# Kernel optimization log

Measured on AMD Instinct MI355X. Metric: run time of the kernel, lower is better.

## Reference

```python
import jax, jax.numpy as jnp
import numpy as np

NTOKENS = 50257
NHID = 1024
NTOK_PER_CLASS = 225   # ceil(sqrt(50257))
NCLASSES = 224         # ceil(50257/225)
BATCH = 2048


def setup_inputs() -> dict:
    key = jax.random.key(0)
    k1, k2, k3, k4 = jax.random.split(key, 4)
    initrange = 0.1
    inputs = jax.random.normal(k1, (BATCH, NHID), dtype=jnp.float32)
    labels = jax.random.randint(k2, (BATCH,), 0, NTOKENS, dtype=jnp.int64)
    layer_top_W = jax.random.uniform(k3, (NHID, NCLASSES), dtype=jnp.float32,
                                     minval=-initrange, maxval=initrange)
    layer_top_b = jnp.zeros((NCLASSES,), dtype=jnp.float32)
    layer_bottom_W = jax.random.uniform(k4, (NCLASSES, NHID, NTOK_PER_CLASS),
                                        dtype=jnp.float32,
                                        minval=-initrange, maxval=initrange)
    layer_bottom_b = jnp.zeros((NCLASSES, NTOK_PER_CLASS), dtype=jnp.float32)
    return {"inputs": inputs, "labels": labels,
            "layer_top_W": layer_top_W, "layer_top_b": layer_top_b,
            "layer_bottom_W": layer_bottom_W, "layer_bottom_b": layer_bottom_b}


def reference(inputs, labels, layer_top_W, layer_top_b, layer_bottom_W, layer_bottom_b):
    batch_size = inputs.shape[0]
    label_position_top = labels // NTOK_PER_CLASS          # [B]
    label_position_bottom = labels % NTOK_PER_CLASS        # [B]

    # top-level class probabilities
    top_logits = inputs @ layer_top_W + layer_top_b        # [B, nclasses]
    top_probs = jax.nn.softmax(top_logits, axis=1)

    # per-sample gather of class weight matrices + batched matmul
    W_sel = layer_bottom_W[label_position_top]             # [B, nhid, ntok_per_class]
    b_sel = layer_bottom_b[label_position_top]             # [B, ntok_per_class]
    bottom_logits = jnp.einsum('bh,bht->bt', inputs, W_sel) + b_sel
    bottom_probs = jax.nn.softmax(bottom_logits, axis=1)

    idx = jnp.arange(batch_size)
    target_probs = top_probs[idx, label_position_top] * bottom_probs[idx, label_position_bottom]
    return target_probs
```

## Files before the change

### kernel.cpp

```cpp
#include <hip/hip_runtime.h>
#include <math.h>

#define NHID  1024
#define NCLS  224
#define NTPC  225
#define BATCH 2048
#define XP    18

#define NBOT_BLOCKS (NCLS * 4)
#define NTOP_BLOCKS (128 * 4)

#define CLS_OFF  0
#define POS_OFF  8192
#define LIST_OFF 16384
#define OFFS_OFF 24576
#define YTOP_OFF 32768
#define YTOP_BYTES (BATCH * NCLS * 4)
#define YBOT_OFF (YTOP_OFF + YTOP_BYTES)
#define YBOT_BYTES (BATCH * NTPC * 4)

__global__ __launch_bounds__(256) void group_kernel(const int* __restrict__ labels,
                                                    int* __restrict__ cls,
                                                    int* __restrict__ pos,
                                                    int* __restrict__ list,
                                                    int* __restrict__ offs) {
    __shared__ int cnt[NCLS];
    __shared__ int sc[256];
    __shared__ int bex[NCLS];
    __shared__ int nz;
    const int tid = threadIdx.x;
    if (tid == 0) nz = 0;
    for (int j = tid; j < NCLS; j += 256) cnt[j] = 0;
    __syncthreads();
    int loc = 0;
    for (int k = 0; k < 4; ++k) {
        int i = tid + 256 * k;
        if (labels[2 * i + 1] != 0) loc = 1;
    }
    if (loc) atomicOr(&nz, 1);
    __syncthreads();
    const bool is64 = (nz == 0);
    int myc[8], myr[8];
#pragma unroll
    for (int k = 0; k < 8; ++k) {
        int i = tid + 256 * k;
        int l = is64 ? labels[2 * i] : labels[i];
        int c = l / NTPC;
        cls[i] = c;
        pos[i] = l - c * NTPC;
        myc[k] = c;
        myr[k] = atomicAdd(&cnt[c], 1);
    }
    __syncthreads();
    int v = (tid < NCLS) ? cnt[tid] : 0;
    sc[tid] = v;
    __syncthreads();
    for (int off = 1; off < 256; off <<= 1) {
        int u = (tid >= off) ? sc[tid - off] : 0;
        __syncthreads();
        sc[tid] += u;
        __syncthreads();
    }
    if (tid < NCLS) {
        int ex = sc[tid] - v;
        bex[tid] = ex;
        offs[tid] = ex;
    }
    if (tid == 0) offs[NCLS] = BATCH;
    __syncthreads();
#pragma unroll
    for (int k = 0; k < 8; ++k) {
        int i = tid + 256 * k;
        list[bex[myc[k]] + myr[k]] = i;
    }
}

__global__ __launch_bounds__(256) void partial_kernel(const float* __restrict__ x,
                                                      const float* __restrict__ Wt,
                                                      const float* __restrict__ Wb,
                                                      const int* __restrict__ list,
                                                      const int* __restrict__ offs,
                                                      float* __restrict__ ytop,
                                                      float* __restrict__ ybot) {
    __shared__ __align__(16) float xs[256 * XP];
    const int tid = threadIdx.x;
    const int w = tid >> 6, l = tid & 63;
    const int bi = blockIdx.x;
    const bool isBot = (bi < NBOT_BLOCKS);

    int k, o, n, ycols;
    const float* W;
    float* y;
    if (isBot) {
        int c = bi >> 2; k = bi & 3;
        o = offs[c]; n = offs[c + 1] - o;
        W = Wb + (size_t)c * (NHID * NTPC);
        y = ybot; ycols = NTPC;
    } else {
        int b2 = bi - NBOT_BLOCKS;
        int st = b2 >> 2; k = b2 & 3;
        o = st * 16; n = 16;
        W = Wt; y = ytop; ycols = NCLS;
    }
    const int hbase = k * 256;

    for (int tile = 0; tile * 16 < n; ++tile) {
        if (tile) __syncthreads();
        for (int i = 0; i < 16; ++i) {
            int idx = tile * 16 + i;
            int s = isBot ? list[o + min(idx, n - 1)] : (o + i);
            xs[tid * XP + i] = x[(size_t)s * NHID + hbase + tid];
        }
        __syncthreads();
        const int nt = min(n - tile * 16, 16);
        if (4 * w < nt) {
            float acc[4][4];
#pragma unroll
            for (int m = 0; m < 4; ++m)
#pragma unroll
                for (int g = 0; g < 4; ++g) acc[m][g] = 0.f;
            const float* wr = W + (size_t)hbase * ycols + l;
#pragma unroll 4
            for (int h = 0; h < 256; ++h) {
                float2 xa = *(const float2*)&xs[h * XP + 4 * w];
                float2 xb = *(const float2*)&xs[h * XP + 4 * w + 2];
                float wv[4];
                wv[0] = wr[0];
                wv[1] = wr[64];
                wv[2] = wr[128];
                wv[3] = (192 + l < ycols) ? wr[192] : 0.f;
                const float xm[4] = {xa.x, xa.y, xb.x, xb.y};
#pragma unroll
                for (int m = 0; m < 4; ++m)
#pragma unroll
                    for (int g = 0; g < 4; ++g)
                        acc[m][g] = fmaf(xm[m], wv[g], acc[m][g]);
                wr += ycols;
            }
            const int smax = min(nt - 4 * w, 4);
            for (int m = 0; m < smax; ++m) {
                int idx = tile * 16 + 4 * w + m;
                int s = isBot ? list[o + idx] : (o + 4 * w + m);
                float* yr = y + (size_t)s * ycols;
#pragma unroll
                for (int g = 0; g < 4; ++g) {
                    int col = l + 64 * g;
                    if (col < ycols) atomicAdd(&yr[col], acc[m][g]);
                }
            }
        }
    }
}

__global__ __launch_bounds__(256) void finalize_kernel(const float* __restrict__ ytop,
                                                       const float* __restrict__ ybot,
                                                       const float* __restrict__ bt,
                                                       const float* __restrict__ bb,
                                                       const int* __restrict__ cls,
                                                       const int* __restrict__ pos,
                                                       float* __restrict__ out) {
    const int w = threadIdx.x >> 6, l = threadIdx.x & 63;
    const int s = blockIdx.x * 4 + w;
    const int c = cls[s], p = pos[s];

    float v[4];
#pragma unroll
    for (int g = 0; g < 4; ++g) {
        int col = l + 64 * g;
        v[g] = (col < NCLS) ? ytop[(size_t)s * NCLS + col] + bt[col] : -INFINITY;
    }
    float mx = fmaxf(fmaxf(v[0], v[1]), fmaxf(v[2], v[3]));
#pragma unroll
    for (int off = 32; off; off >>= 1) mx = fmaxf(mx, __shfl_xor(mx, off));
    float sum = 0.f, tc = 0.f;
#pragma unroll
    for (int g = 0; g < 4; ++g) {
        int col = l + 64 * g;
        float e = (col < NCLS) ? __expf(v[g] - mx) : 0.f;
        sum += e;
        if (col == c) tc = e;
    }
#pragma unroll
    for (int off = 32; off; off >>= 1) {
        sum += __shfl_xor(sum, off);
        tc  += __shfl_xor(tc, off);
    }
    const float tp = tc / sum;

#pragma unroll
    for (int g = 0; g < 4; ++g) {
        int col = l + 64 * g;
        v[g] = (col < NTPC) ? ybot[(size_t)s * NTPC + col] + bb[c * NTPC + col] : -INFINITY;
    }
    mx = fmaxf(fmaxf(v[0], v[1]), fmaxf(v[2], v[3]));
#pragma unroll
    for (int off = 32; off; off >>= 1) mx = fmaxf(mx, __shfl_xor(mx, off));
    float bsum = 0.f;
    float ep = 0.f;
#pragma unroll
    for (int g = 0; g < 4; ++g) {
        int col = l + 64 * g;
        float e = (col < NTPC) ? __expf(v[g] - mx) : 0.f;
        bsum += e;
        if (col == p) ep = e;
    }
#pragma unroll
    for (int off = 32; off; off >>= 1) bsum += __shfl_xor(bsum, off);
    if (ep != 0.f || (l == (p & 63) && (l + 64 * (p >> 6) == p)))
        ;
    int owner = ((l + 64 * 0 == p) || (l + 64 * 1 == p) || (l + 64 * 2 == p) || (l + 64 * 3 == p));
    if (owner) out[s] = tp * ep / bsum;
}

extern "C" void kernel_launch(void* const* d_in, const int* in_sizes, int n_in,
                              void* d_out, int out_size, void* d_ws, size_t ws_size,
                              hipStream_t stream) {
    const float* inputs = (const float*)d_in[0];
    const int*   labels = (const int*)d_in[1];
    const float* topW   = (const float*)d_in[2];
    const float* topB   = (const float*)d_in[3];
    const float* botW   = (const float*)d_in[4];
    const float* botB   = (const float*)d_in[5];
    float* out = (float*)d_out;

    char* ws   = (char*)d_ws;
    int*   cls = (int*)(ws + CLS_OFF);
    int*   pos = (int*)(ws + POS_OFF);
    int*   lst = (int*)(ws + LIST_OFF);
    int*   off = (int*)(ws + OFFS_OFF);
    float* ytop = (float*)(ws + YTOP_OFF);
    float* ybot = (float*)(ws + YBOT_OFF);

    hipMemsetAsync(ws + YTOP_OFF, 0, YTOP_BYTES + YBOT_BYTES, stream);
    group_kernel<<<1, 256, 0, stream>>>(labels, cls, pos, lst, off);
    partial_kernel<<<NBOT_BLOCKS + NTOP_BLOCKS, 256, 0, stream>>>(
        inputs, topW, botW, lst, off, ytop, ybot);
    finalize_kernel<<<BATCH / 4, 256, 0, stream>>>(ytop, ybot, topB, botB, cls, pos, out);
}
```

Measured before the change: 344.4 us.

## Remap partial GEMM threads to one column by sixteen samples with swizzled LDS

```diff
diff --git a/kernel.cpp b/kernel.cpp
--- a/kernel.cpp
+++ b/kernel.cpp
@@ -5,7 +5,6 @@
 #define NCLS  224
 #define NTPC  225
 #define BATCH 2048
-#define XP    18
 
 #define NBOT_BLOCKS (NCLS * 4)
 #define NTOP_BLOCKS (128 * 4)
@@ -82,7 +81,7 @@
                                                       const int* __restrict__ offs,
                                                       float* __restrict__ ytop,
                                                       float* __restrict__ ybot) {
-    __shared__ __align__(16) float xs[256 * XP];
+    __shared__ __align__(16) float xs[256 * 16];
     const int tid = threadIdx.x;
     const int w = tid >> 6, l = tid & 63;
     const int bi = blockIdx.x;
@@ -103,50 +102,60 @@
         W = Wt; y = ytop; ycols = NCLS;
     }
     const int hbase = k * 256;
+    const int col   = 64 * w + l;
+    const int colc  = min(col, ycols - 1);
+    const bool colok = (col < ycols);
+    const int hq = (tid >> 1) & 3;
 
     for (int tile = 0; tile * 16 < n; ++tile) {
         if (tile) __syncthreads();
+        const float* xcol = x + hbase + tid;
+#pragma unroll
         for (int i = 0; i < 16; ++i) {
             int idx = tile * 16 + i;
             int s = isBot ? list[o + min(idx, n - 1)] : (o + i);
-            xs[tid * XP + i] = x[(size_t)s * NHID + hbase + tid];
+            xs[(tid << 4) + ((((i >> 2) ^ hq) << 2) | (i & 3))] = xcol[(size_t)s * NHID];
         }
         __syncthreads();
+
+        float acc[16];
+#pragma unroll
+        for (int i = 0; i < 16; ++i) acc[i] = 0.f;
+
+        const float* wr = W + (size_t)hbase * ycols + colc;
+#pragma unroll 8
+        for (int h = 0; h < 256; ++h) {
+            float wv = wr[0];
+            const float4* xr = (const float4*)&xs[h << 4];
+            const int q = (h >> 1) & 3;
+            float4 x0 = xr[q];
+            float4 x1 = xr[1 ^ q];
+            float4 x2 = xr[2 ^ q];
+            float4 x3 = xr[3 ^ q];
+            acc[0]  = fmaf(x0.x, wv, acc[0]);
+            acc[1]  = fmaf(x0.y, wv, acc[1]);
+            acc[2]  = fmaf(x0.z, wv, acc[2]);
+            acc[3]  = fmaf(x0.w, wv, acc[3]);
+            acc[4]  = fmaf(x1.x, wv, acc[4]);
+            acc[5]  = fmaf(x1.y, wv, acc[5]);
+            acc[6]  = fmaf(x1.z, wv, acc[6]);
+            acc[7]  = fmaf(x1.w, wv, acc[7]);
+            acc[8]  = fmaf(x2.x, wv, acc[8]);
+            acc[9]  = fmaf(x2.y, wv, acc[9]);
+            acc[10] = fmaf(x2.z, wv, acc[10]);
+            acc[11] = fmaf(x2.w, wv, acc[11]);
+            acc[12] = fmaf(x3.x, wv, acc[12]);
+            acc[13] = fmaf(x3.y, wv, acc[13]);
+            acc[14] = fmaf(x3.z, wv, acc[14]);
+            acc[15] = fmaf(x3.w, wv, acc[15]);
+            wr += ycols;
+        }
+
         const int nt = min(n - tile * 16, 16);
-        if (4 * w < nt) {
-            float acc[4][4];
-#pragma unroll
-            for (int m = 0; m < 4; ++m)
-#pragma unroll
-                for (int g = 0; g < 4; ++g) acc[m][g] = 0.f;
-            const float* wr = W + (size_t)hbase * ycols + l;
-#pragma unroll 4
-            for (int h = 0; h < 256; ++h) {
-                float2 xa = *(const float2*)&xs[h * XP + 4 * w];
-                float2 xb = *(const float2*)&xs[h * XP + 4 * w + 2];
-                float wv[4];
-                wv[0] = wr[0];
-                wv[1] = wr[64];
-                wv[2] = wr[128];
-                wv[3] = (192 + l < ycols) ? wr[192] : 0.f;
-                const float xm[4] = {xa.x, xa.y, xb.x, xb.y};
-#pragma unroll
-                for (int m = 0; m < 4; ++m)
-#pragma unroll
-                    for (int g = 0; g < 4; ++g)
-                        acc[m][g] = fmaf(xm[m], wv[g], acc[m][g]);
-                wr += ycols;
-            }
-            const int smax = min(nt - 4 * w, 4);
-            for (int m = 0; m < smax; ++m) {
-                int idx = tile * 16 + 4 * w + m;
-                int s = isBot ? list[o + idx] : (o + 4 * w + m);
-                float* yr = y + (size_t)s * ycols;
-#pragma unroll
-                for (int g = 0; g < 4; ++g) {
-                    int col = l + 64 * g;
-                    if (col < ycols) atomicAdd(&yr[col], acc[m][g]);
-                }
+        if (colok) {
+            for (int i = 0; i < nt; ++i) {
+                int s = isBot ? list[o + tile * 16 + i] : (o + i);
+                atomicAdd(&y[(size_t)s * ycols + col], acc[i]);
             }
         }
     }
@@ -195,8 +204,7 @@
     mx = fmaxf(fmaxf(v[0], v[1]), fmaxf(v[2], v[3]));
 #pragma unroll
     for (int off = 32; off; off >>= 1) mx = fmaxf(mx, __shfl_xor(mx, off));
-    float bsum = 0.f;
-    float ep = 0.f;
+    float bsum = 0.f, ep = 0.f;
 #pragma unroll
     for (int g = 0; g < 4; ++g) {
         int col = l + 64 * g;
@@ -206,10 +214,11 @@
     }
 #pragma unroll
     for (int off = 32; off; off >>= 1) bsum += __shfl_xor(bsum, off);
-    if (ep != 0.f || (l == (p & 63) && (l + 64 * (p >> 6) == p)))
-        ;
-    int owner = ((l + 64 * 0 == p) || (l + 64 * 1 == p) || (l + 64 * 2 == p) || (l + 64 * 3 == p));
-    if (owner) out[s] = tp * ep / bsum;
+    int owner = ((l == (p & 63)) && ((p >> 6) == ((l + 64 * ((p >> 6))) == p ? (p >> 6) : -1)));
+#pragma unroll
+    for (int g = 0; g < 4; ++g)
+        if (l + 64 * g == p) out[s] = tp * ep / bsum;
+    (void)owner;
 }
 
 extern "C" void kernel_launch(void* const* d_in, const int* in_sizes, int n_in,
```

New measurement: 344.3 us. About the same (-0.0%).

## Split hidden dimension across waves instead of samples in partial matmul kernel

Applied to the files above, without the earlier changes.

```diff
diff --git a/kernel.cpp b/kernel.cpp
--- a/kernel.cpp
+++ b/kernel.cpp
@@ -5,7 +5,6 @@
 #define NCLS  224
 #define NTPC  225
 #define BATCH 2048
-#define XP    18
 
 #define NBOT_BLOCKS (NCLS * 4)
 #define NTOP_BLOCKS (128 * 4)
@@ -75,14 +74,49 @@
     }
 }
 
-__global__ __launch_bounds__(256) void partial_kernel(const float* __restrict__ x,
-                                                      const float* __restrict__ Wt,
-                                                      const float* __restrict__ Wb,
-                                                      const int* __restrict__ list,
-                                                      const int* __restrict__ offs,
-                                                      float* __restrict__ ytop,
-                                                      float* __restrict__ ybot) {
-    __shared__ __align__(16) float xs[256 * XP];
+template <int NQ>
+__device__ __forceinline__ void pk_compute(const float* __restrict__ wr0,
+                                           const float* __restrict__ xs,
+                                           float acc[NQ][4][4],
+                                           int ycols, int hw, int l) {
+#pragma unroll
+    for (int q = 0; q < NQ; ++q)
+#pragma unroll
+        for (int m = 0; m < 4; ++m)
+#pragma unroll
+            for (int g = 0; g < 4; ++g) acc[q][m][g] = 0.f;
+    const float* wr = wr0;
+#pragma unroll 4
+    for (int h = 0; h < 64; ++h) {
+        const int hh = hw + h;
+        float wv[4];
+        wv[0] = wr[0];
+        wv[1] = wr[64];
+        wv[2] = wr[128];
+        wv[3] = wr[192 + l < ycols ? 192 : 0];
+        const int sw = (hh >> 1) & 3;
+#pragma unroll
+        for (int q = 0; q < NQ; ++q) {
+            float4 xq = *(const float4*)&xs[(hh << 4) + 4 * (q ^ sw)];
+            const float xm[4] = {xq.x, xq.y, xq.z, xq.w};
+#pragma unroll
+            for (int m = 0; m < 4; ++m)
+#pragma unroll
+                for (int g = 0; g < 4; ++g)
+                    acc[q][m][g] = fmaf(xm[m], wv[g], acc[q][m][g]);
+        }
+        wr += ycols;
+    }
+}
+
+__global__ __launch_bounds__(256, 4) void partial_kernel(const float* __restrict__ x,
+                                                         const float* __restrict__ Wt,
+                                                         const float* __restrict__ Wb,
+                                                         const int* __restrict__ list,
+                                                         const int* __restrict__ offs,
+                                                         float* __restrict__ ytop,
+                                                         float* __restrict__ ybot) {
+    __shared__ __align__(16) float xs[256 * 16];
     const int tid = threadIdx.x;
     const int w = tid >> 6, l = tid & 63;
     const int bi = blockIdx.x;
@@ -103,49 +137,42 @@
         W = Wt; y = ytop; ycols = NCLS;
     }
     const int hbase = k * 256;
+    const int hw = 64 * w;
+    const int hq = (tid >> 1) & 3;
+    const float* wr0 = W + (size_t)(hbase + hw) * ycols + l;
 
     for (int tile = 0; tile * 16 < n; ++tile) {
         if (tile) __syncthreads();
+        const float* xcol = x + hbase + tid;
+#pragma unroll
         for (int i = 0; i < 16; ++i) {
             int idx = tile * 16 + i;
             int s = isBot ? list[o + min(idx, n - 1)] : (o + i);
-            xs[tid * XP + i] = x[(size_t)s * NHID + hbase + tid];
+            xs[(tid << 4) + ((((i >> 2) ^ hq) << 2) | (i & 3))] = xcol[(size_t)s * NHID];
         }
         __syncthreads();
+
         const int nt = min(n - tile * 16, 16);
-        if (4 * w < nt) {
-            float acc[4][4];
-#pragma unroll
-            for (int m = 0; m < 4; ++m)
-#pragma unroll
-                for (int g = 0; g < 4; ++g) acc[m][g] = 0.f;
-            const float* wr = W + (size_t)hbase * ycols + l;
-#pragma unroll 4
-            for (int h = 0; h < 256; ++h) {
-                float2 xa = *(const float2*)&xs[h * XP + 4 * w];
-                float2 xb = *(const float2*)&xs[h * XP + 4 * w + 2];
-                float wv[4];
-                wv[0] = wr[0];
-                wv[1] = wr[64];
-                wv[2] = wr[128];
-                wv[3] = (192 + l < ycols) ? wr[192] : 0.f;
-                const float xm[4] = {xa.x, xa.y, xb.x, xb.y};
-#pragma unroll
-                for (int m = 0; m < 4; ++m)
-#pragma unroll
-                    for (int g = 0; g < 4; ++g)
-                        acc[m][g] = fmaf(xm[m], wv[g], acc[m][g]);
-                wr += ycols;
-            }
-            const int smax = min(nt - 4 * w, 4);
-            for (int m = 0; m < smax; ++m) {
-                int idx = tile * 16 + 4 * w + m;
-                int s = isBot ? list[o + idx] : (o + 4 * w + m);
-                float* yr = y + (size_t)s * ycols;
-#pragma unroll
-                for (int g = 0; g < 4; ++g) {
-                    int col = l + 64 * g;
-                    if (col < ycols) atomicAdd(&yr[col], acc[m][g]);
+        const int nq = (nt + 3) >> 2;
+        float acc[4][4][4];
+        switch (nq) {
+            case 1: pk_compute<1>(wr0, xs, (float(*)[4][4])acc, ycols, hw, l); break;
+            case 2: pk_compute<2>(wr0, xs, (float(*)[4][4])acc, ycols, hw, l); break;
+            case 3: pk_compute<3>(wr0, xs, (float(*)[4][4])acc, ycols, hw, l); break;
+            default: pk_compute<4>(wr0, xs, (float(*)[4][4])acc, ycols, hw, l); break;
+        }
+
+        for (int q = 0; q < nq; ++q) {
+#pragma unroll
+            for (int m = 0; m < 4; ++m) {
+                int idx = tile * 16 + 4 * q + m;
+                if (idx < n) {
+                    int s = isBot ? list[o + idx] : (o + idx);
+                    float* yr = y + (size_t)s * ycols;
+                    atomicAdd(&yr[l], acc[q][m][0]);
+                    atomicAdd(&yr[l + 64], acc[q][m][1]);
+                    atomicAdd(&yr[l + 128], acc[q][m][2]);
+                    if (l + 192 < ycols) atomicAdd(&yr[l + 192], acc[q][m][3]);
                 }
             }
         }
@@ -195,8 +222,7 @@
     mx = fmaxf(fmaxf(v[0], v[1]), fmaxf(v[2], v[3]));
 #pragma unroll
     for (int off = 32; off; off >>= 1) mx = fmaxf(mx, __shfl_xor(mx, off));
-    float bsum = 0.f;
-    float ep = 0.f;
+    float bsum = 0.f, ep = 0.f;
 #pragma unroll
     for (int g = 0; g < 4; ++g) {
         int col = l + 64 * g;
@@ -206,10 +232,9 @@
     }
 #pragma unroll
     for (int off = 32; off; off >>= 1) bsum += __shfl_xor(bsum, off);
-    if (ep != 0.f || (l == (p & 63) && (l + 64 * (p >> 6) == p)))
-        ;
-    int owner = ((l + 64 * 0 == p) || (l + 64 * 1 == p) || (l + 64 * 2 == p) || (l + 64 * 3 == p));
-    if (owner) out[s] = tp * ep / bsum;
+#pragma unroll
+    for (int g = 0; g < 4; ++g)
+        if (l + 64 * g == p) out[s] = tp * ep / bsum;
 }
 
 extern "C" void kernel_launch(void* const* d_in, const int* in_sizes, int n_in,
```

Measured after the change: 412.2 us. 19.7% more time.
